# Kernel tuning notes

Hardware: AMD Instinct MI355X
Metric: run time of the kernel (lower is better)

## Reference

```python
import jax, jax.numpy as jnp
import numpy as np

SINKHORN_ALPHA = 20.0
WEIGHT_LOSS_ECR = 100.0
OT_MAX_ITER = 100
STOP_THR = 0.005
EPS = 1e-16


def setup_inputs() -> dict:
    key = jax.random.key(0)
    # cost matrix: topics x vocab, nonnegative
    M = jax.random.uniform(key, (2000, 20000), dtype=jnp.float32)
    return {"M": M}


def reference(M):
    n, m = M.shape
    a = jnp.full((n, 1), 1.0 / n, dtype=M.dtype)  # uniform row marginal
    b = jnp.full((m, 1), 1.0 / m, dtype=M.dtype)  # uniform col marginal
    K = jnp.exp(-M * SINKHORN_ALPHA)              # Gibbs kernel, (n, m)

    u0 = jnp.full((n, 1), 1.0 / n, dtype=M.dtype)
    v0 = jnp.zeros((m, 1), dtype=M.dtype)
    err0 = jnp.asarray(1.0, dtype=M.dtype)
    cpt0 = jnp.asarray(0, dtype=jnp.int32)

    def cond(carry):
        u, v, err, cpt = carry
        return (err > STOP_THR) & (cpt < OT_MAX_ITER)

    def body(carry):
        u, v, err, cpt = carry
        v = b / (K.T @ u + EPS)          # (m, 1)
        u = a / (K @ v + EPS)            # (n, 1)
        cpt = cpt + 1
        # convergence check every 50 iterations (cpt % 50 == 1), as in torch
        bb = v * (K.T @ u)               # (m, 1) implied col marginal
        err_new = jnp.max(jnp.sum(jnp.abs(bb - b), axis=0))
        err = jnp.where(cpt % 50 == 1, err_new.astype(err.dtype), err)
        return (u, v, err, cpt)

    u, v, err, cpt = jax.lax.while_loop(cond, body, (u0, v0, err0, cpt0))

    transp = u * (K * v.T)               # transport plan, (n, m)
    loss_ECR = jnp.sum(transp * M)
    return loss_ECR * WEIGHT_LOSS_ECR
```

## Files before the change

### kernel.cpp

```cpp
#include <hip/hip_runtime.h>
#include <hip/hip_fp16.h>

typedef unsigned int uint32;
typedef float floatx2 __attribute__((ext_vector_type(2)));

#define ROWS_R 2000
#define COLS_R 20000
#define ROWS_P 2048
#define COLS_P 20480
#define DWC_P  (COLS_P/4)
#define DWR_P  (ROWS_P/4)
#define NBLK   256
#define NTHR   1024
#define NWAVE  16
#define TSTRIDE 132

static constexpr float A_MARG = 1.0f / 2000.0f;
static constexpr float B_MARG = 1.0f / 20000.0f;
static constexpr float EPSV   = 1e-16f;
static constexpr float THR    = 0.005f;
static constexpr float NALPHA = -20.0f;

__device__ __forceinline__ void grid_barrier(uint32* ctrl, uint32 rnd) {
    __syncthreads();
    if (threadIdx.x == 0) {
        const int gid = (int)(blockIdx.x >> 5);
        uint32* gcnt = ctrl + 128 + gid * 64;
        uint32* ggen = ctrl + 768 + gid * 64;
        __threadfence();
        uint32 a = __hip_atomic_fetch_add(gcnt, 1u, __ATOMIC_RELAXED, __HIP_MEMORY_SCOPE_AGENT);
        if (a == rnd * 32u + 31u) {
            uint32 r = __hip_atomic_fetch_add(ctrl, 1u, __ATOMIC_RELAXED, __HIP_MEMORY_SCOPE_AGENT);
            if (r == rnd * 8u + 7u) {
                __hip_atomic_fetch_add(ctrl + 64, 1u, __ATOMIC_RELAXED, __HIP_MEMORY_SCOPE_AGENT);
            } else {
                while (__hip_atomic_load(ctrl + 64, __ATOMIC_RELAXED, __HIP_MEMORY_SCOPE_AGENT) < rnd + 1u)
                    __builtin_amdgcn_s_sleep(1);
            }
            __hip_atomic_fetch_add(ggen, 1u, __ATOMIC_RELAXED, __HIP_MEMORY_SCOPE_AGENT);
        } else {
            while (__hip_atomic_load(ggen, __ATOMIC_RELAXED, __HIP_MEMORY_SCOPE_AGENT) < rnd + 1u)
                __builtin_amdgcn_s_sleep(1);
        }
        __threadfence();
    }
    __syncthreads();
}

__global__ __launch_bounds__(256) void init_kernel(float* __restrict__ u_g,
                                                   uint32* __restrict__ ctrl,
                                                   float* __restrict__ err2,
                                                   float* __restrict__ loss) {
    int idx = blockIdx.x * 256 + threadIdx.x;
    if (idx < 1280) ctrl[idx] = 0u;
    if (idx == 0) { err2[0] = 0.f; err2[1] = 0.f; *loss = 0.f; }
    if (idx < 2048) u_g[idx] = (idx < ROWS_R) ? A_MARG : 0.0f;
}

__global__ __launch_bounds__(NTHR, 1) void sinkhorn_fused(
    const float*  __restrict__ M,
    uint32* __restrict__ Krm,
    uint32* __restrict__ Kcm,
    float* __restrict__ u_g,
    float* __restrict__ v_g,
    uint32* __restrict__ ctrl,
    float* __restrict__ err2,
    float* __restrict__ loss,
    float* __restrict__ out) {
    __shared__ float  s_v[COLS_P];
    __shared__ uint32 T[64 * TSTRIDE];
    __shared__ float  s_red[NWAVE * 4];
    __shared__ int    s_flag;

    const int tid  = threadIdx.x;
    const int lane = tid & 63;
    const int wav  = tid >> 6;
    const int b    = blockIdx.x;
    uint32 bar = 0;

    {
        const int fx  = tid & 15;
        const int ry  = tid >> 4;
        const int xsw = fx & 3;
        for (int tt = 0; tt < 5; ++tt) {
            const int tile  = b * 5 + tt;
            const int c64   = tile % 320;
            const int chunk = tile / 320;
            const int c0    = c64 * 64;
            const int col   = c0 + fx * 4;
#pragma unroll
            for (int s = 0; s < 2; ++s) {
                const int rq = s * 64 + ry;
                uint32 kd[4];
#pragma unroll
                for (int i = 0; i < 4; ++i) {
                    const int r = chunk * 512 + rq * 4 + i;
                    uint32 pack = 0u;
                    if (r < ROWS_R && col < COLS_R) {
                        float4 m = *reinterpret_cast<const float4*>(M + (size_t)r * COLS_R + col);
                        float k0 = __expf(NALPHA * m.x), k1 = __expf(NALPHA * m.y);
                        float k2 = __expf(NALPHA * m.z), k3 = __expf(NALPHA * m.w);
                        int lo = __builtin_amdgcn_cvt_pk_fp8_f32(k0, k1, 0, false);
                        int hi = __builtin_amdgcn_cvt_pk_fp8_f32(k2, k3, lo, true);
                        pack = (uint32)hi;
                    }
                    kd[i] = pack;
                    Krm[(size_t)(chunk * 512 + rq * 4 + i) * DWC_P + (c0 >> 2) + fx] = pack;
                }
                uint32 x0 = __builtin_amdgcn_perm(kd[1], kd[0], 0x05010400u);
                uint32 x1 = __builtin_amdgcn_perm(kd[1], kd[0], 0x07030602u);
                uint32 x2 = __builtin_amdgcn_perm(kd[3], kd[2], 0x05010400u);
                uint32 x3 = __builtin_amdgcn_perm(kd[3], kd[2], 0x07030602u);
                uint32 o0 = __builtin_amdgcn_perm(x2, x0, 0x05040100u);
                uint32 o1 = __builtin_amdgcn_perm(x2, x0, 0x07060302u);
                uint32 o2 = __builtin_amdgcn_perm(x3, x1, 0x05040100u);
                uint32 o3 = __builtin_amdgcn_perm(x3, x1, 0x07060302u);
                const int rqs = rq ^ (xsw << 2);
                T[(4 * fx + 0) * TSTRIDE + rqs] = o0;
                T[(4 * fx + 1) * TSTRIDE + rqs] = o1;
                T[(4 * fx + 2) * TSTRIDE + rqs] = o2;
                T[(4 * fx + 3) * TSTRIDE + rqs] = o3;
            }
            __syncthreads();
#pragma unroll
            for (int k = 0; k < 2; ++k) {
                const int idx   = k * 1024 + tid;
                const int col_l = idx >> 5;
                const int m4    = idx & 31;
                const int mm    = m4 ^ ((col_l >> 2) & 3);
                uint4 d = *reinterpret_cast<const uint4*>(&T[col_l * TSTRIDE + 4 * mm]);
                *reinterpret_cast<uint4*>(Kcm + (size_t)(c0 + col_l) * DWR_P + chunk * 128 + 4 * m4) = d;
            }
            __syncthreads();
        }
    }
    grid_barrier(ctrl, bar++);

    const float4* u_g4 = reinterpret_cast<const float4*>(u_g);

    for (int t = 1; t <= 100; ++t) {
        const bool chk = (t == 2) || (t == 52);
        const int  slot = (t == 52) ? 1 : 0;

        float4 u_r[8];
#pragma unroll
        for (int s = 0; s < 8; ++s) u_r[s] = u_g4[s * 64 + lane];

        float e = 0.f;
#pragma unroll
        for (int q = 0; q < 5; ++q) {
            const int j = b * 80 + wav * 5 + q;
            const uint32* colp = Kcm + (size_t)j * DWR_P;
            float acc = 0.f;
#pragma unroll
            for (int s = 0; s < 8; ++s) {
                uint32 kw = colp[s * 64 + lane];
                floatx2 f01 = __builtin_amdgcn_cvt_pk_f32_fp8(kw, false);
                floatx2 f23 = __builtin_amdgcn_cvt_pk_f32_fp8(kw, true);
                acc += f01.x * u_r[s].x + f01.y * u_r[s].y + f23.x * u_r[s].z + f23.y * u_r[s].w;
            }
#pragma unroll
            for (int o = 32; o; o >>= 1) acc += __shfl_xor(acc, o, 64);
            if (lane == 0) {
                v_g[j] = B_MARG / (acc + EPSV);
                if (chk && j < COLS_R) e += fabsf(s_v[j] * acc - B_MARG);
            }
        }
        if (chk) {
            if (lane == 0) s_red[wav] = e;
            __syncthreads();
            if (tid == 0) {
                float s = 0.f;
                for (int k = 0; k < NWAVE; ++k) s += s_red[k];
                if (s != 0.f) atomicAdd(&err2[slot], s);
            }
        }
        grid_barrier(ctrl, bar++);

        if (chk) {
            if (tid == 0) s_flag = (err2[slot] <= THR) ? 1 : 0;
            __syncthreads();
            if (s_flag) break;
        }

        {
            float4* d = reinterpret_cast<float4*>(s_v);
            const float4* srcv = reinterpret_cast<const float4*>(v_g);
#pragma unroll
            for (int k = 0; k < 5; ++k) d[k * 1024 + tid] = srcv[k * 1024 + tid];
        }
        __syncthreads();

        {
            const int rq = wav >> 3;
            const int sg = wav & 7;
            const int rbase = b * 8 + rq * 4;
            const uint32* kp  = Krm + (size_t)rbase * DWC_P + sg * 640;
            const float4* sv4 = reinterpret_cast<const float4*>(s_v) + sg * 640;
            float acc0 = 0.f, acc1 = 0.f, acc2 = 0.f, acc3 = 0.f;
#pragma unroll 2
            for (int s = 0; s < 10; ++s) {
                const int idx = s * 64 + lane;
                float4 vv = sv4[idx];
                uint32 k0 = kp[idx];
                uint32 k1 = kp[idx + DWC_P];
                uint32 k2 = kp[idx + 2 * DWC_P];
                uint32 k3 = kp[idx + 3 * DWC_P];
                floatx2 a0 = __builtin_amdgcn_cvt_pk_f32_fp8(k0, false);
                floatx2 b0 = __builtin_amdgcn_cvt_pk_f32_fp8(k0, true);
                acc0 += a0.x * vv.x + a0.y * vv.y + b0.x * vv.z + b0.y * vv.w;
                floatx2 a1 = __builtin_amdgcn_cvt_pk_f32_fp8(k1, false);
                floatx2 b1 = __builtin_amdgcn_cvt_pk_f32_fp8(k1, true);
                acc1 += a1.x * vv.x + a1.y * vv.y + b1.x * vv.z + b1.y * vv.w;
                floatx2 a2 = __builtin_amdgcn_cvt_pk_f32_fp8(k2, false);
                floatx2 b2 = __builtin_amdgcn_cvt_pk_f32_fp8(k2, true);
                acc2 += a2.x * vv.x + a2.y * vv.y + b2.x * vv.z + b2.y * vv.w;
                floatx2 a3 = __builtin_amdgcn_cvt_pk_f32_fp8(k3, false);
                floatx2 b3 = __builtin_amdgcn_cvt_pk_f32_fp8(k3, true);
                acc3 += a3.x * vv.x + a3.y * vv.y + b3.x * vv.z + b3.y * vv.w;
            }
#pragma unroll
            for (int o = 32; o; o >>= 1) {
                acc0 += __shfl_xor(acc0, o, 64);
                acc1 += __shfl_xor(acc1, o, 64);
                acc2 += __shfl_xor(acc2, o, 64);
                acc3 += __shfl_xor(acc3, o, 64);
            }
            if (lane == 0) {
                s_red[wav * 4 + 0] = acc0;
                s_red[wav * 4 + 1] = acc1;
                s_red[wav * 4 + 2] = acc2;
                s_red[wav * 4 + 3] = acc3;
            }
        }
        __syncthreads();
        if (tid < 8) {
            const int row = b * 8 + tid;
            if (row < ROWS_R) {
                const int rq2 = tid >> 2, i = tid & 3;
                float s = 0.f;
#pragma unroll
                for (int sg = 0; sg < 8; ++sg) s += s_red[(rq2 * 8 + sg) * 4 + i];
                u_g[row] = A_MARG / (s + EPSV);
            }
        }
        grid_barrier(ctrl, bar++);
    }

    {
        const float4* sv4 = reinterpret_cast<const float4*>(s_v);
        const int rw = b * NWAVE + wav;
        if (rw < ROWS_R) {
            const float4* mrow = reinterpret_cast<const float4*>(M + (size_t)rw * COLS_R);
            float acc = 0.f;
            for (int ci = lane; ci < 5000; ci += 64) {
                float4 m = mrow[ci];
                float4 vv = sv4[ci];
                acc += __expf(NALPHA * m.x) * vv.x * m.x;
                acc += __expf(NALPHA * m.y) * vv.y * m.y;
                acc += __expf(NALPHA * m.z) * vv.z * m.z;
                acc += __expf(NALPHA * m.w) * vv.w * m.w;
            }
#pragma unroll
            for (int o = 32; o; o >>= 1) acc += __shfl_xor(acc, o, 64);
            if (lane == 0) atomicAdd(loss, acc * u_g[rw]);
        }
    }
    grid_barrier(ctrl, bar++);
    if (b == 0 && tid == 0) out[0] = *loss * 100.0f;
}


__device__ __forceinline__ float block_reduce_sum256(float v) {
#pragma unroll
    for (int o = 32; o; o >>= 1) v += __shfl_down(v, o, 64);
    __shared__ float smem[4];
    int lane = threadIdx.x & 63, w = threadIdx.x >> 6;
    if (lane == 0) smem[w] = v;
    __syncthreads();
    v = (threadIdx.x < 4) ? smem[threadIdx.x] : 0.0f;
    v += __shfl_down(v, 2, 64);
    v += __shfl_down(v, 1, 64);
    return v;
}

__global__ __launch_bounds__(256) void fb_init(float* u, float* vden, int* done, float* err, float* loss) {
    int idx = blockIdx.x * 256 + threadIdx.x;
    if (idx == 0) { *done = 0; *err = 0.0f; *loss = 0.0f; }
    if (idx < ROWS_R) u[idx] = A_MARG;
    if (idx < COLS_R) vden[idx] = 0.0f;
}
__global__ __launch_bounds__(256) void fb_colpass(const float* __restrict__ M, const float* __restrict__ u,
                                                  float* __restrict__ vden, const int* __restrict__ done) {
    if (*done) return;
    int c4 = blockIdx.x * 256 + threadIdx.x;
    if (c4 >= 5000) return;
    int r0 = blockIdx.y * 50;
    float4 acc = make_float4(0.f, 0.f, 0.f, 0.f);
    for (int r = r0; r < r0 + 50; ++r) {
        float ui = u[r];
        float4 mm = reinterpret_cast<const float4*>(M)[(size_t)r * 5000 + c4];
        acc.x += __expf(NALPHA * mm.x) * ui; acc.y += __expf(NALPHA * mm.y) * ui;
        acc.z += __expf(NALPHA * mm.z) * ui; acc.w += __expf(NALPHA * mm.w) * ui;
    }
    atomicAdd(&vden[c4 * 4 + 0], acc.x); atomicAdd(&vden[c4 * 4 + 1], acc.y);
    atomicAdd(&vden[c4 * 4 + 2], acc.z); atomicAdd(&vden[c4 * 4 + 3], acc.w);
}
__global__ __launch_bounds__(256) void fb_finv(float* v, float* vden, const int* done) {
    if (*done) return;
    int j = blockIdx.x * 256 + threadIdx.x;
    if (j < COLS_R) { v[j] = B_MARG / (vden[j] + EPSV); vden[j] = 0.0f; }
}
__global__ __launch_bounds__(256) void fb_rowpass(const float* __restrict__ M, const float* __restrict__ v,
                                                  float* __restrict__ u, const int* __restrict__ done) {
    if (*done) return;
    int row = blockIdx.x;
    const float4* v4 = reinterpret_cast<const float4*>(v);
    float acc = 0.0f;
    for (int c4 = threadIdx.x; c4 < 5000; c4 += 256) {
        float4 mm = reinterpret_cast<const float4*>(M)[(size_t)row * 5000 + c4];
        float4 vv = v4[c4];
        acc += __expf(NALPHA * mm.x) * vv.x + __expf(NALPHA * mm.y) * vv.y
             + __expf(NALPHA * mm.z) * vv.z + __expf(NALPHA * mm.w) * vv.w;
    }
    float s = block_reduce_sum256(acc);
    if (threadIdx.x == 0) u[row] = A_MARG / (s + EPSV);
}
__global__ __launch_bounds__(256) void fb_errfin(const float* v, float* vden, float* err, const int* done) {
    if (*done) return;
    int j = blockIdx.x * 256 + threadIdx.x;
    float local = 0.0f;
    if (j < COLS_R) { local = fabsf(v[j] * vden[j] - B_MARG); vden[j] = 0.0f; }
    float s = block_reduce_sum256(local);
    if (threadIdx.x == 0) atomicAdd(err, s);
}
__global__ void fb_check(int* done, float* err) {
    if (threadIdx.x == 0) { if (!*done && *err <= THR) *done = 1; *err = 0.0f; }
}
__global__ __launch_bounds__(256) void fb_loss(const float* __restrict__ M, const float* __restrict__ u,
                                               const float* __restrict__ v, float* __restrict__ loss) {
    int row = blockIdx.x;
    const float4* M4p = reinterpret_cast<const float4*>(M + (size_t)row * COLS_R);
    const float4* v4 = reinterpret_cast<const float4*>(v);
    float acc = 0.0f;
    for (int c4 = threadIdx.x; c4 < 5000; c4 += 256) {
        float4 mm = M4p[c4]; float4 vv = v4[c4];
        acc += __expf(NALPHA * mm.x) * vv.x * mm.x + __expf(NALPHA * mm.y) * vv.y * mm.y
             + __expf(NALPHA * mm.z) * vv.z * mm.z + __expf(NALPHA * mm.w) * vv.w * mm.w;
    }
    float s = block_reduce_sum256(acc);
    if (threadIdx.x == 0) atomicAdd(loss, s * u[row]);
}
__global__ void fb_writeout(float* out, const float* loss) {
    if (threadIdx.x == 0) out[0] = *loss * 100.0f;
}


extern "C" void kernel_launch(void* const* d_in, const int* in_sizes, int n_in,
                              void* d_out, int out_size, void* d_ws, size_t ws_size,
                              hipStream_t stream) {
    const float* M = (const float*)d_in[0];
    char* base = (char*)d_ws;

    const size_t OFF_CTRL = 0;
    const size_t OFF_ERR  = 8192;
    const size_t OFF_LOSS = 8320;
    const size_t OFF_U    = 8448;
    const size_t OFF_V    = OFF_U + 8192;
    const size_t OFF_KRM  = OFF_V + 81920;
    const size_t K_BYTES  = (size_t)ROWS_P * COLS_P;
    const size_t OFF_KCM  = OFF_KRM + K_BYTES;
    const size_t NEED     = OFF_KCM + K_BYTES;

    if (ws_size >= NEED) {
        uint32* ctrl = (uint32*)(base + OFF_CTRL);
        float*  err2 = (float*)(base + OFF_ERR);
        float*  loss = (float*)(base + OFF_LOSS);
        float*  u_g  = (float*)(base + OFF_U);
        float*  v_g  = (float*)(base + OFF_V);
        uint32* Krm  = (uint32*)(base + OFF_KRM);
        uint32* Kcm  = (uint32*)(base + OFF_KCM);

        init_kernel<<<8, 256, 0, stream>>>(u_g, ctrl, err2, loss);
        sinkhorn_fused<<<NBLK, NTHR, 0, stream>>>(M, Krm, Kcm, u_g, v_g,
                                                  ctrl, err2, loss, (float*)d_out);
    } else {
        int*   done = (int*)(base + 0);
        float* err  = (float*)(base + 8);
        float* loss = (float*)(base + 16);
        float* u    = (float*)(base + 64);
        float* v    = (float*)(base + 64 + 8192);
        float* vden = (float*)(base + 64 + 8192 + 80000);

        fb_init<<<79, 256, 0, stream>>>(u, vden, done, err, loss);
        dim3 cgrid(20, 40);
        for (int t = 1; t <= 100; ++t) {
            fb_colpass<<<cgrid, 256, 0, stream>>>(M, u, vden, done);
            fb_finv<<<79, 256, 0, stream>>>(v, vden, done);
            fb_rowpass<<<ROWS_R, 256, 0, stream>>>(M, v, u, done);
            if (t == 1 || t == 51) {
                fb_colpass<<<cgrid, 256, 0, stream>>>(M, u, vden, done);
                fb_errfin<<<79, 256, 0, stream>>>(v, vden, err, done);
                fb_check<<<1, 64, 0, stream>>>(done, err);
            }
        }
        fb_loss<<<ROWS_R, 256, 0, stream>>>(M, u, v, loss);
        fb_writeout<<<1, 64, 0, stream>>>((float*)d_out, loss);
    }
}
```

Measured before the change: 393.3 us.

## Keep per-block column slab of FP8 kernel resident in LDS across iterations

Each block now builds its 80-column slab of the FP8 Gibbs kernel directly in shared memory (about 160KB) and keeps it there for the whole run. This removes the global row-major and column-major K copies and the per-iteration global reads of K. The row pass becomes per-block partial sums written to a global buffer P, which each block then reduces for its 8 rows. The final loss is computed column-slab-wise from the local v. It trades global K traffic for LDS traffic and a cross-block partial-sum exchange, and LDS capacity limits any further restructuring. The column-wise M reads during setup are strided, which may make setup slower.

```diff
diff --git a/kernel.cpp b/kernel.cpp
--- a/kernel.cpp
+++ b/kernel.cpp
@@ -1,19 +1,17 @@
 #include <hip/hip_runtime.h>
-#include <hip/hip_fp16.h>
 
 typedef unsigned int uint32;
 typedef float floatx2 __attribute__((ext_vector_type(2)));
 
 #define ROWS_R 2000
 #define COLS_R 20000
-#define ROWS_P 2048
-#define COLS_P 20480
-#define DWC_P  (COLS_P/4)
-#define DWR_P  (ROWS_P/4)
 #define NBLK   256
 #define NTHR   1024
 #define NWAVE  16
-#define TSTRIDE 132
+#define CPB    80
+#define CSTR   501
+#define KDW    (CPB*CSTR)
+#define KGUARD 16
 
 static constexpr float A_MARG = 1.0f / 2000.0f;
 static constexpr float B_MARG = 1.0f / 20000.0f;
@@ -57,89 +55,52 @@
     if (idx < 2048) u_g[idx] = (idx < ROWS_R) ? A_MARG : 0.0f;
 }
 
-__global__ __launch_bounds__(NTHR, 1) void sinkhorn_fused(
-    const float*  __restrict__ M,
-    uint32* __restrict__ Krm,
-    uint32* __restrict__ Kcm,
+__global__ __launch_bounds__(NTHR, 1) void sinkhorn_lds(
+    const float* __restrict__ M,
     float* __restrict__ u_g,
-    float* __restrict__ v_g,
+    float* __restrict__ P,
     uint32* __restrict__ ctrl,
     float* __restrict__ err2,
     float* __restrict__ loss,
     float* __restrict__ out) {
-    __shared__ float  s_v[COLS_P];
-    __shared__ uint32 T[64 * TSTRIDE];
-    __shared__ float  s_red[NWAVE * 4];
+    __shared__ uint32 sK[KDW + KGUARD];
+    __shared__ float  s_vloc[CPB];
+    __shared__ float  s_vprev[CPB];
+    __shared__ float  s_red[NWAVE * 8];
     __shared__ int    s_flag;
 
     const int tid  = threadIdx.x;
     const int lane = tid & 63;
     const int wav  = tid >> 6;
     const int b    = blockIdx.x;
+    const int j0   = b * CPB;
     uint32 bar = 0;
 
-    {
-        const int fx  = tid & 15;
-        const int ry  = tid >> 4;
-        const int xsw = fx & 3;
-        for (int tt = 0; tt < 5; ++tt) {
-            const int tile  = b * 5 + tt;
-            const int c64   = tile % 320;
-            const int chunk = tile / 320;
-            const int c0    = c64 * 64;
-            const int col   = c0 + fx * 4;
-#pragma unroll
-            for (int s = 0; s < 2; ++s) {
-                const int rq = s * 64 + ry;
-                uint32 kd[4];
-#pragma unroll
-                for (int i = 0; i < 4; ++i) {
-                    const int r = chunk * 512 + rq * 4 + i;
-                    uint32 pack = 0u;
-                    if (r < ROWS_R && col < COLS_R) {
-                        float4 m = *reinterpret_cast<const float4*>(M + (size_t)r * COLS_R + col);
-                        float k0 = __expf(NALPHA * m.x), k1 = __expf(NALPHA * m.y);
-                        float k2 = __expf(NALPHA * m.z), k3 = __expf(NALPHA * m.w);
-                        int lo = __builtin_amdgcn_cvt_pk_fp8_f32(k0, k1, 0, false);
-                        int hi = __builtin_amdgcn_cvt_pk_fp8_f32(k2, k3, lo, true);
-                        pack = (uint32)hi;
-                    }
-                    kd[i] = pack;
-                    Krm[(size_t)(chunk * 512 + rq * 4 + i) * DWC_P + (c0 >> 2) + fx] = pack;
-                }
-                uint32 x0 = __builtin_amdgcn_perm(kd[1], kd[0], 0x05010400u);
-                uint32 x1 = __builtin_amdgcn_perm(kd[1], kd[0], 0x07030602u);
-                uint32 x2 = __builtin_amdgcn_perm(kd[3], kd[2], 0x05010400u);
-                uint32 x3 = __builtin_amdgcn_perm(kd[3], kd[2], 0x07030602u);
-                uint32 o0 = __builtin_amdgcn_perm(x2, x0, 0x05040100u);
-                uint32 o1 = __builtin_amdgcn_perm(x2, x0, 0x07060302u);
-                uint32 o2 = __builtin_amdgcn_perm(x3, x1, 0x05040100u);
-                uint32 o3 = __builtin_amdgcn_perm(x3, x1, 0x07060302u);
-                const int rqs = rq ^ (xsw << 2);
-                T[(4 * fx + 0) * TSTRIDE + rqs] = o0;
-                T[(4 * fx + 1) * TSTRIDE + rqs] = o1;
-                T[(4 * fx + 2) * TSTRIDE + rqs] = o2;
-                T[(4 * fx + 3) * TSTRIDE + rqs] = o3;
-            }
-            __syncthreads();
-#pragma unroll
-            for (int k = 0; k < 2; ++k) {
-                const int idx   = k * 1024 + tid;
-                const int col_l = idx >> 5;
-                const int m4    = idx & 31;
-                const int mm    = m4 ^ ((col_l >> 2) & 3);
-                uint4 d = *reinterpret_cast<const uint4*>(&T[col_l * TSTRIDE + 4 * mm]);
-                *reinterpret_cast<uint4*>(Kcm + (size_t)(c0 + col_l) * DWR_P + chunk * 128 + 4 * m4) = d;
-            }
-            __syncthreads();
-        }
-    }
-    grid_barrier(ctrl, bar++);
+    for (int i = tid; i < KDW + KGUARD; i += NTHR) sK[i] = 0u;
+    __syncthreads();
+    for (int q = wav; q < 500; q += NWAVE) {
+#pragma unroll
+        for (int ph = 0; ph < 2; ++ph) {
+            const int cl = ph * 64 + lane;
+            const int j  = j0 + cl;
+            if ((ph == 0 || lane < 16) && j < COLS_R) {
+                const float* mp = M + (size_t)(4 * q) * COLS_R + j;
+                float k0 = __expf(NALPHA * mp[0]);
+                float k1 = __expf(NALPHA * mp[COLS_R]);
+                float k2 = __expf(NALPHA * mp[2 * COLS_R]);
+                float k3 = __expf(NALPHA * mp[3 * COLS_R]);
+                int lo = __builtin_amdgcn_cvt_pk_fp8_f32(k0, k1, 0, false);
+                int hi = __builtin_amdgcn_cvt_pk_fp8_f32(k2, k3, lo, true);
+                sK[cl * CSTR + q] = (uint32)hi;
+            }
+        }
+    }
+    __syncthreads();
 
     const float4* u_g4 = reinterpret_cast<const float4*>(u_g);
 
     for (int t = 1; t <= 100; ++t) {
-        const bool chk = (t == 2) || (t == 52);
+        const bool chk  = (t == 2) || (t == 52);
         const int  slot = (t == 52) ? 1 : 0;
 
         float4 u_r[8];
@@ -149,12 +110,11 @@
         float e = 0.f;
 #pragma unroll
         for (int q = 0; q < 5; ++q) {
-            const int j = b * 80 + wav * 5 + q;
-            const uint32* colp = Kcm + (size_t)j * DWR_P;
+            const int jl = wav * 5 + q;
             float acc = 0.f;
 #pragma unroll
             for (int s = 0; s < 8; ++s) {
-                uint32 kw = colp[s * 64 + lane];
+                uint32 kw = sK[jl * CSTR + s * 64 + lane];
                 floatx2 f01 = __builtin_amdgcn_cvt_pk_f32_fp8(kw, false);
                 floatx2 f23 = __builtin_amdgcn_cvt_pk_f32_fp8(kw, true);
                 acc += f01.x * u_r[s].x + f01.y * u_r[s].y + f23.x * u_r[s].z + f23.y * u_r[s].w;
@@ -162,108 +122,95 @@
 #pragma unroll
             for (int o = 32; o; o >>= 1) acc += __shfl_xor(acc, o, 64);
             if (lane == 0) {
-                v_g[j] = B_MARG / (acc + EPSV);
-                if (chk && j < COLS_R) e += fabsf(s_v[j] * acc - B_MARG);
-            }
-        }
-        if (chk) {
-            if (lane == 0) s_red[wav] = e;
-            __syncthreads();
-            if (tid == 0) {
-                float s = 0.f;
-                for (int k = 0; k < NWAVE; ++k) s += s_red[k];
-                if (s != 0.f) atomicAdd(&err2[slot], s);
-            }
+                float vnew = B_MARG / (acc + EPSV);
+                if (chk) {
+                    float vold = s_vloc[jl];
+                    s_vprev[jl] = vold;
+                    if (j0 + jl < COLS_R) e += fabsf(vold * acc - B_MARG);
+                }
+                s_vloc[jl] = vnew;
+            }
+        }
+        if (chk && lane == 0) s_red[wav] = e;
+        __syncthreads();
+
+        float4 pa = make_float4(0.f, 0.f, 0.f, 0.f);
+#pragma unroll 8
+        for (int jp = 0; jp < 40; ++jp) {
+            const int cl = 2 * jp + (lane >> 5);
+            const int m  = lane & 31;
+            uint32 kw = sK[cl * CSTR + wav * 32 + m];
+            float  vv = s_vloc[cl];
+            floatx2 f01 = __builtin_amdgcn_cvt_pk_f32_fp8(kw, false);
+            floatx2 f23 = __builtin_amdgcn_cvt_pk_f32_fp8(kw, true);
+            pa.x += f01.x * vv; pa.y += f01.y * vv;
+            pa.z += f23.x * vv; pa.w += f23.y * vv;
+        }
+        pa.x += __shfl_xor(pa.x, 32, 64);
+        pa.y += __shfl_xor(pa.y, 32, 64);
+        pa.z += __shfl_xor(pa.z, 32, 64);
+        pa.w += __shfl_xor(pa.w, 32, 64);
+        if (lane < 32)
+            *reinterpret_cast<float4*>(P + (size_t)b * 2048 + wav * 128 + 4 * lane) = pa;
+
+        if (chk && tid == 0) {
+            float s = 0.f;
+            for (int k = 0; k < NWAVE; ++k) s += s_red[k];
+            if (s != 0.f) atomicAdd(&err2[slot], s);
         }
         grid_barrier(ctrl, bar++);
 
         if (chk) {
             if (tid == 0) s_flag = (err2[slot] <= THR) ? 1 : 0;
             __syncthreads();
-            if (s_flag) break;
+            if (s_flag) {
+                if (tid < CPB) s_vloc[tid] = s_vprev[tid];
+                __syncthreads();
+                break;
+            }
         }
 
         {
-            float4* d = reinterpret_cast<float4*>(s_v);
-            const float4* srcv = reinterpret_cast<const float4*>(v_g);
-#pragma unroll
-            for (int k = 0; k < 5; ++k) d[k * 1024 + tid] = srcv[k * 1024 + tid];
-        }
-        __syncthreads();
-
-        {
-            const int rq = wav >> 3;
-            const int sg = wav & 7;
-            const int rbase = b * 8 + rq * 4;
-            const uint32* kp  = Krm + (size_t)rbase * DWC_P + sg * 640;
-            const float4* sv4 = reinterpret_cast<const float4*>(s_v) + sg * 640;
-            float acc0 = 0.f, acc1 = 0.f, acc2 = 0.f, acc3 = 0.f;
-#pragma unroll 2
-            for (int s = 0; s < 10; ++s) {
-                const int idx = s * 64 + lane;
-                float4 vv = sv4[idx];
-                uint32 k0 = kp[idx];
-                uint32 k1 = kp[idx + DWC_P];
-                uint32 k2 = kp[idx + 2 * DWC_P];
-                uint32 k3 = kp[idx + 3 * DWC_P];
-                floatx2 a0 = __builtin_amdgcn_cvt_pk_f32_fp8(k0, false);
-                floatx2 b0 = __builtin_amdgcn_cvt_pk_f32_fp8(k0, true);
-                acc0 += a0.x * vv.x + a0.y * vv.y + b0.x * vv.z + b0.y * vv.w;
-                floatx2 a1 = __builtin_amdgcn_cvt_pk_f32_fp8(k1, false);
-                floatx2 b1 = __builtin_amdgcn_cvt_pk_f32_fp8(k1, true);
-                acc1 += a1.x * vv.x + a1.y * vv.y + b1.x * vv.z + b1.y * vv.w;
-                floatx2 a2 = __builtin_amdgcn_cvt_pk_f32_fp8(k2, false);
-                floatx2 b2 = __builtin_amdgcn_cvt_pk_f32_fp8(k2, true);
-                acc2 += a2.x * vv.x + a2.y * vv.y + b2.x * vv.z + b2.y * vv.w;
-                floatx2 a3 = __builtin_amdgcn_cvt_pk_f32_fp8(k3, false);
-                floatx2 b3 = __builtin_amdgcn_cvt_pk_f32_fp8(k3, true);
-                acc3 += a3.x * vv.x + a3.y * vv.y + b3.x * vv.z + b3.y * vv.w;
-            }
-#pragma unroll
-            for (int o = 32; o; o >>= 1) {
-                acc0 += __shfl_xor(acc0, o, 64);
-                acc1 += __shfl_xor(acc1, o, 64);
-                acc2 += __shfl_xor(acc2, o, 64);
-                acc3 += __shfl_xor(acc3, o, 64);
-            }
-            if (lane == 0) {
-                s_red[wav * 4 + 0] = acc0;
-                s_red[wav * 4 + 1] = acc1;
-                s_red[wav * 4 + 2] = acc2;
-                s_red[wav * 4 + 3] = acc3;
-            }
+            float v0 = P[(size_t)(tid >> 3) * 2048 + 8 * b + (tid & 7)];
+            float v1 = P[(size_t)((tid >> 3) + 128) * 2048 + 8 * b + (tid & 7)];
+            float s = v0 + v1;
+            s += __shfl_xor(s, 8, 64);
+            s += __shfl_xor(s, 16, 64);
+            s += __shfl_xor(s, 32, 64);
+            if (lane < 8) s_red[wav * 8 + lane] = s;
         }
         __syncthreads();
         if (tid < 8) {
-            const int row = b * 8 + tid;
-            if (row < ROWS_R) {
-                const int rq2 = tid >> 2, i = tid & 3;
-                float s = 0.f;
-#pragma unroll
-                for (int sg = 0; sg < 8; ++sg) s += s_red[(rq2 * 8 + sg) * 4 + i];
-                u_g[row] = A_MARG / (s + EPSV);
-            }
+            float s = 0.f;
+            for (int w = 0; w < NWAVE; ++w) s += s_red[w * 8 + tid];
+            const int row = 8 * b + tid;
+            u_g[row] = (row < ROWS_R) ? A_MARG / (s + EPSV) : 0.0f;
         }
         grid_barrier(ctrl, bar++);
     }
 
     {
-        const float4* sv4 = reinterpret_cast<const float4*>(s_v);
-        const int rw = b * NWAVE + wav;
-        if (rw < ROWS_R) {
-            const float4* mrow = reinterpret_cast<const float4*>(M + (size_t)rw * COLS_R);
-            float acc = 0.f;
-            for (int ci = lane; ci < 5000; ci += 64) {
-                float4 m = mrow[ci];
-                float4 vv = sv4[ci];
-                acc += __expf(NALPHA * m.x) * vv.x * m.x;
-                acc += __expf(NALPHA * m.y) * vv.y * m.y;
-                acc += __expf(NALPHA * m.z) * vv.z * m.z;
-                acc += __expf(NALPHA * m.w) * vv.w * m.w;
-            }
-#pragma unroll
-            for (int o = 32; o; o >>= 1) acc += __shfl_xor(acc, o, 64);
-            if (lane == 0) atomicAdd(loss, acc * u_g[rw]);
+        float acc = 0.f;
+        for (int r = wav; r < ROWS_R; r += NWAVE) {
+            const float uu = u_g[r];
+            const float* mp = M + (size_t)r * COLS_R + j0;
+#pragma unroll
+            for (int ph = 0; ph < 2; ++ph) {
+                const int cl = ph * 64 + lane;
+                if ((ph == 0 || lane < 16) && (j0 + cl) < COLS_R) {
+                    float m = mp[cl];
+                    acc += uu * __expf(NALPHA * m) * s_vloc[cl] * m;
+                }
+            }
+        }
+#pragma unroll
+        for (int o = 32; o; o >>= 1) acc += __shfl_xor(acc, o, 64);
+        if (lane == 0) s_red[wav] = acc;
+        __syncthreads();
+        if (tid == 0) {
+            float s = 0.f;
+            for (int k = 0; k < NWAVE; ++k) s += s_red[k];
+            if (s != 0.f) atomicAdd(loss, s);
         }
     }
     grid_barrier(ctrl, bar++);
@@ -366,24 +313,18 @@
     const size_t OFF_ERR  = 8192;
     const size_t OFF_LOSS = 8320;
     const size_t OFF_U    = 8448;
-    const size_t OFF_V    = OFF_U + 8192;
-    const size_t OFF_KRM  = OFF_V + 81920;
-    const size_t K_BYTES  = (size_t)ROWS_P * COLS_P;
-    const size_t OFF_KCM  = OFF_KRM + K_BYTES;
-    const size_t NEED     = OFF_KCM + K_BYTES;
+    const size_t OFF_P    = OFF_U + 8192 + 256;
+    const size_t NEED     = OFF_P + (size_t)NBLK * 2048 * 4;
 
     if (ws_size >= NEED) {
         uint32* ctrl = (uint32*)(base + OFF_CTRL);
         float*  err2 = (float*)(base + OFF_ERR);
         float*  loss = (float*)(base + OFF_LOSS);
         float*  u_g  = (float*)(base + OFF_U);
-        float*  v_g  = (float*)(base + OFF_V);
-        uint32* Krm  = (uint32*)(base + OFF_KRM);
-        uint32* Kcm  = (uint32*)(base + OFF_KCM);
+        float*  P    = (float*)(base + OFF_P);
 
         init_kernel<<<8, 256, 0, stream>>>(u_g, ctrl, err2, loss);
-        sinkhorn_fused<<<NBLK, NTHR, 0, stream>>>(M, Krm, Kcm, u_g, v_g,
-                                                  ctrl, err2, loss, (float*)d_out);
+        sinkhorn_lds<<<NBLK, NTHR, 0, stream>>>(M, u_g, P, ctrl, err2, loss, (float*)d_out);
     } else {
         int*   done = (int*)(base + 0);
         float* err  = (float*)(base + 8);
```

Result: faster. 365.7 us (-7.0%).
